# Performance work log

Hardware: AMD Instinct MI355X
Metric: run time of the kernel (lower is better)

## Reference

```python
import math
import jax, jax.numpy as jnp
import numpy as np

D_HEAD = 64
KS = 7
EPS = 1e-6


def _rope_freqs(d_head, n_heads):
    # AxialRoPE buffer: exp(linspace(log(pi), log(10*pi), nh*dim//4+1)[:-1]).view(dim//4, nh).T
    dim = d_head // 2
    n = n_heads * dim // 4
    f = np.exp(np.linspace(math.log(math.pi), math.log(10.0 * math.pi), n + 1)[:-1]).astype(np.float32)
    return jnp.asarray(f.reshape(dim // 4, n_heads).T)  # [nh, dim//4]


def setup_inputs() -> dict:
    key = jax.random.key(0)
    ks = jax.random.split(key, 6)
    B, C, T, H, W = 1, 512, 4, 32, 32
    cond_features = 256
    nh = C // D_HEAD
    x = jax.random.normal(ks[0], (B, C, T, H, W), dtype=jnp.float32)
    pos = jax.random.uniform(ks[1], (B, H, W, 2), dtype=jnp.float32)
    cond = jax.random.normal(ks[2], (B, cond_features), dtype=jnp.float32)
    # zero-init layers in the original (norm.linear, out_proj) get small random weights
    # here so the reference exercises nontrivial math/gradients.
    norm_w = jax.random.normal(ks[3], (cond_features, C), dtype=jnp.float32) * 0.02
    qkv_w = jax.random.normal(ks[4], (C, 3 * C), dtype=jnp.float32) * (1.0 / math.sqrt(C))
    out_w = jax.random.normal(ks[5], (C, C), dtype=jnp.float32) * (1.0 / math.sqrt(C))
    scale = jnp.full((nh,), 10.0, dtype=jnp.float32)
    return {"x": x, "pos": pos, "cond": cond, "norm_w": norm_w, "qkv_w": qkv_w,
            "scale": scale, "out_w": out_w}


def reference(x, pos, cond, norm_w, qkv_w, scale, out_w):
    B, C, T, H, W = x.shape
    nh = C // D_HEAD
    N = B * T
    skip = x

    # b c t h w -> (b t) h w c
    xr = jnp.transpose(x, (0, 2, 3, 4, 1)).reshape(N, H, W, C)
    condr = jnp.repeat(cond, T, axis=0)  # (b t) c, b-major

    # AdaRMSNorm: scale = linear(cond) + 1, applied with rms normalization
    s = condr @ norm_w + 1.0  # [N, C]
    mean_sq = jnp.mean(xr * xr, axis=-1, keepdims=True)
    xn = xr * (s[:, None, None, :] * jax.lax.rsqrt(mean_sq + EPS))

    qkv = (xn @ qkv_w).reshape(N, H, W, 3, nh, D_HEAD)
    q, k, v = qkv[:, :, :, 0], qkv[:, :, :, 1], qkv[:, :, :, 2]  # [N,H,W,nh,e]

    # cosine-sim scaling per head
    sqrt_scale = jnp.sqrt(scale)[:, None]  # [nh,1]
    q = q * (sqrt_scale * jax.lax.rsqrt(jnp.sum(q * q, -1, keepdims=True) + EPS))
    k = k * (sqrt_scale * jax.lax.rsqrt(jnp.sum(k * k, -1, keepdims=True) + EPS))

    # axial RoPE
    freqs = _rope_freqs(D_HEAD, nh)  # [nh, e//8]
    theta = jnp.concatenate([pos[..., None, 0:1] * freqs,
                             pos[..., None, 1:2] * freqs], axis=-1)  # [B,H,W,nh,e//4]
    theta = jnp.repeat(theta, T, axis=0)  # [N,H,W,nh,d]
    d = theta.shape[-1]
    cos_t, sin_t = jnp.cos(theta), jnp.sin(theta)

    def rope(t):
        x1, x2, x3 = t[..., :d], t[..., d:2 * d], t[..., 2 * d:]
        return jnp.concatenate([x1 * cos_t - x2 * sin_t,
                                x2 * cos_t + x1 * sin_t, x3], axis=-1)

    q, k = rope(q), rope(k)

    # neighborhood attention (NATTEN na2d semantics: window clamped to image border)
    r = KS // 2
    ih = jnp.clip(jnp.arange(H) - r, 0, H - KS)[:, None] + jnp.arange(KS)  # [H,KS]
    iw = jnp.clip(jnp.arange(W) - r, 0, W - KS)[:, None] + jnp.arange(KS)  # [W,KS]

    def windows(t):  # [N,H,W,nh,e] -> [N,H,W,KS*KS,nh,e]
        g = t[:, ih[:, :, None, None], iw[None, None, :, :]]  # [N,H,KS,W,KS,nh,e]
        return jnp.transpose(g, (0, 1, 3, 2, 4, 5, 6)).reshape(N, H, W, KS * KS, nh, D_HEAD)

    kw, vw = windows(k), windows(v)
    logits = jnp.einsum('nhwce,nhwkce->nhwck', q, kw)  # scale=1.0 in na2d call
    attn = jax.nn.softmax(logits, axis=-1)
    o = jnp.einsum('nhwck,nhwkce->nhwce', attn, vw).reshape(N, H, W, C)

    y = o @ out_w  # dropout=0.0
    y = jnp.transpose(y.reshape(B, T, H, W, C), (0, 4, 1, 2, 3))
    return y + skip
```

## Files before the change

kernel.cpp:

```cpp
#include <hip/hip_runtime.h>
#include <hip/hip_bf16.h>

typedef __hip_bfloat16 bf16;
#define F32(b) __bfloat162float(b)
#define B16(f) __float2bfloat16(f)

typedef __attribute__((ext_vector_type(8))) short short8;
typedef __attribute__((ext_vector_type(4))) float f32x4;

#define C_DIM 512
#define P_DIM 4096

__device__ __forceinline__ float wave_sum(float v){
#pragma unroll
  for (int o = 32; o > 0; o >>= 1) v += __shfl_xor(v, o, 64);
  return v;
}

__global__ __launch_bounds__(256) void k_prep_s(const float* __restrict__ cond,
                                                const float* __restrict__ norm_w,
                                                float* __restrict__ s){
  __shared__ float red[8][33];
  int c_l = threadIdx.x & 31, fo = threadIdx.x >> 5;
  int c = blockIdx.x * 32 + c_l;
  float acc = 0.f;
  for (int f = fo * 32; f < fo * 32 + 32; ++f)
    acc = fmaf(cond[f], norm_w[f * 512 + c], acc);
  red[fo][c_l] = acc;
  __syncthreads();
  if (threadIdx.x < 32){
    float a = 0.f;
#pragma unroll
    for (int i = 0; i < 8; ++i) a += red[i][c_l];
    s[blockIdx.x * 32 + c_l] = a + 1.0f;
  }
}

__global__ __launch_bounds__(256) void k_rms(const float* __restrict__ x,
                                             float* __restrict__ rms_part){
  __shared__ float red[4][64];
  int bp = blockIdx.x & 63, bc = blockIdx.x >> 6;
  int co = threadIdx.x >> 6, pl = threadIdx.x & 63;
  int p = bp * 64 + pl;
  float acc = 0.f;
  for (int c = bc * 64 + co; c < bc * 64 + 64; c += 4){
    float v = x[c * P_DIM + p];
    acc = fmaf(v, v, acc);
  }
  red[co][pl] = acc;
  __syncthreads();
  if (threadIdx.x < 64){
    int q = threadIdx.x;
    rms_part[bc * P_DIM + bp * 64 + q] = red[0][q] + red[1][q] + red[2][q] + red[3][q];
  }
}

__global__ __launch_bounds__(256) void k_castwT(const float* __restrict__ qkv_w,
                                                const float* __restrict__ out_w,
                                                bf16* __restrict__ qkvT,
                                                bf16* __restrict__ outT){
  __shared__ float tile[64][65];
  int bid = blockIdx.x;
  const float* src; bf16* dst; int NW, n0, c0;
  if (bid < 192){ src = qkv_w; dst = qkvT; NW = 1536; n0 = (bid % 24) * 64; c0 = (bid / 24) * 64; }
  else { int b = bid - 192; src = out_w; dst = outT; NW = 512; n0 = (b & 7) * 64; c0 = (b >> 3) * 64; }
  int grp = threadIdx.x >> 6, lane = threadIdx.x & 63;
  for (int i = grp; i < 64; i += 4)
    tile[i][lane] = src[(c0 + i) * NW + n0 + lane];
  __syncthreads();
  for (int j = grp; j < 64; j += 4)
    dst[(n0 + j) * 512 + c0 + lane] = B16(tile[lane][j]);
}

__global__ __launch_bounds__(256) void k_xnt(const float* __restrict__ x,
                                             const float* __restrict__ s,
                                             const float* __restrict__ rms_part,
                                             bf16* __restrict__ xn){
  __shared__ float tile[64][65];
  int bp = blockIdx.x & 63, bc = blockIdx.x >> 6;
  int p0 = bp * 64, c0 = bc * 64;
  int grp = threadIdx.x >> 6, lane = threadIdx.x & 63;
  for (int i = grp; i < 64; i += 4)
    tile[i][lane] = x[(c0 + i) * P_DIM + p0 + lane] * s[c0 + i];
  __syncthreads();
  for (int j = grp; j < 64; j += 4){
    float ss = 0.f;
#pragma unroll
    for (int i = 0; i < 8; ++i) ss += rms_part[i * P_DIM + p0 + j];
    float rv = rsqrtf(ss * (1.0f / 512.0f) + 1e-6f);
    xn[(size_t)(p0 + j) * 512 + c0 + lane] = B16(tile[lane][j] * rv);
  }
}

#define AS 72
__global__ __launch_bounds__(256) void k_gemm_qkv(const bf16* __restrict__ Ab,
                                                  const bf16* __restrict__ BTb,
                                                  bf16* __restrict__ qkv_bf){
  __shared__ unsigned short a_t[128 * AS];
  __shared__ unsigned short b_t[64 * AS];
  const unsigned short* A  = (const unsigned short*)Ab;
  const unsigned short* BT = (const unsigned short*)BTb;
  int m0 = blockIdx.x * 128;
  int n0 = blockIdx.y * 64;
  int tid = threadIdx.x;
  int w = tid >> 6, l = tid & 63, g = l >> 4, cb = l & 15;

  f32x4 acc[2][4];
#pragma unroll
  for (int mi = 0; mi < 2; ++mi)
#pragma unroll
    for (int nj = 0; nj < 4; ++nj)
#pragma unroll
      for (int r = 0; r < 4; ++r) acc[mi][nj][r] = 0.f;

  for (int kk = 0; kk < 512; kk += 64){
#pragma unroll
    for (int i = 0; i < 4; ++i){
      int sid = tid + i * 256;
      int row = sid >> 3, seg = sid & 7;
      *(uint4*)&a_t[row * AS + seg * 8] = *(const uint4*)&A[(size_t)(m0 + row) * 512 + kk + seg * 8];
    }
#pragma unroll
    for (int i = 0; i < 2; ++i){
      int sid = tid + i * 256;
      int row = sid >> 3, seg = sid & 7;
      *(uint4*)&b_t[row * AS + seg * 8] = *(const uint4*)&BT[(size_t)(n0 + row) * 512 + kk + seg * 8];
    }
    __syncthreads();
#pragma unroll
    for (int kc = 0; kc < 2; ++kc){
      short8 af[2];
#pragma unroll
      for (int mi = 0; mi < 2; ++mi)
        af[mi] = *(const short8*)&a_t[(w * 32 + mi * 16 + cb) * AS + kc * 32 + g * 8];
#pragma unroll
      for (int nj = 0; nj < 4; ++nj){
        short8 bfr = *(const short8*)&b_t[(nj * 16 + cb) * AS + kc * 32 + g * 8];
#pragma unroll
        for (int mi = 0; mi < 2; ++mi)
          acc[mi][nj] = __builtin_amdgcn_mfma_f32_16x16x32_bf16(af[mi], bfr, acc[mi][nj], 0, 0, 0);
      }
    }
    __syncthreads();
  }
#pragma unroll
  for (int mi = 0; mi < 2; ++mi)
#pragma unroll
    for (int nj = 0; nj < 4; ++nj){
      int col = n0 + nj * 16 + cb;
#pragma unroll
      for (int r = 0; r < 4; ++r){
        int rowg = m0 + w * 32 + mi * 16 + g * 4 + r;
        qkv_bf[(size_t)rowg * 1536 + col] = B16(acc[mi][nj][r]);
      }
    }
}

__global__ __launch_bounds__(256) void k_normrope(bf16* __restrict__ qkv_bf,
                                                  const float* __restrict__ scale,
                                                  const float* __restrict__ pos){
  int u = blockIdx.x * 4 + (threadIdx.x >> 6);
  int d = threadIdx.x & 63;
  int p = u >> 4;
  int r = u & 15;
  int head = r >> 1;
  int qk = r & 1;
  size_t base = (size_t)p * 1536 + qk * 512 + head * 64;
  float v = F32(qkv_bf[base + d]);
  float ss = wave_sum(v * v);
  v *= sqrtf(scale[head]) * rsqrtf(ss + 1e-6f);
  float partner = __shfl_xor(v, 16, 64);
  int j = d & 15;
  int axis = j >> 3, i = j & 7;
  const float LOG_PI = 1.1447298858494002f;
  const float LOG10F = 2.302585092994046f;
  float f = __expf(LOG_PI + (float)(i * 8 + head) * (LOG10F / 64.0f));
  float th = pos[(p & 1023) * 2 + axis] * f;
  float ct = __cosf(th), st = __sinf(th);
  float outv;
  if (d < 16)       outv = v * ct - partner * st;
  else if (d < 32)  outv = v * ct + partner * st;
  else              outv = v;
  qkv_bf[base + d] = B16(outv);
}

#define KL_S 80
#define VT_S 232
#define PP_S 232
__global__ __launch_bounds__(256) void k_attn(const bf16* __restrict__ qkv_bfp,
                                              bf16* __restrict__ o_bf){
  __shared__ unsigned short kp[208 * KL_S];
  __shared__ unsigned short vT[64 * VT_S];
  const unsigned short* qkv = (const unsigned short*)qkv_bfp;

  int bid = blockIdx.x;
  int head = bid & 7;
  int patch = bid >> 3;
  int t = patch >> 4;
  int ph = (patch >> 2) & 3, pw = patch & 3;
  int h0 = ph * 8, w0 = pw * 8;
  int rs = min(max(h0 - 3, 0), 18);
  int cs = min(max(w0 - 3, 0), 18);
  int tbase = t << 10;
  int tid = threadIdx.x;
  int cp = tid & 31, pxg = tid >> 5;

  for (int i = 0; i < 26; ++i){
    int px = i * 8 + pxg;
    unsigned val = 0;
    if (px < 196){
      int rr = px / 14, cc = px - rr * 14;
      size_t pn = (size_t)(tbase + (rs + rr) * 32 + (cs + cc));
      val = *(const unsigned*)&qkv[pn * 1536 + 512 + head * 64 + cp * 2];
    }
    *(unsigned*)&kp[px * KL_S + cp * 2] = val;
  }
  for (int i = 0; i < 14; ++i){
    int pp = i * 8 + pxg;
    int px0 = 2 * pp, px1 = px0 + 1;
    unsigned v0 = 0, v1 = 0;
    if (px0 < 196){
      int rr = px0 / 14, cc = px0 - rr * 14;
      size_t pn = (size_t)(tbase + (rs + rr) * 32 + (cs + cc));
      v0 = *(const unsigned*)&qkv[pn * 1536 + 1024 + head * 64 + cp * 2];
    }
    if (px1 < 196){
      int rr = px1 / 14, cc = px1 - rr * 14;
      size_t pn = (size_t)(tbase + (rs + rr) * 32 + (cs + cc));
      v1 = *(const unsigned*)&qkv[pn * 1536 + 1024 + head * 64 + cp * 2];
    }
    unsigned lo = (v0 & 0xffffu) | (v1 << 16);
    unsigned hi = (v0 >> 16) | (v1 & 0xffff0000u);
    *(unsigned*)&vT[(2 * cp) * VT_S + 2 * pp] = lo;
    *(unsigned*)&vT[(2 * cp + 1) * VT_S + 2 * pp] = hi;
  }

  int w = tid >> 6, l = tid & 63;
  int g = l >> 4, cb = l & 15;

  int q_a = w * 16 + cb;
  size_t abase = (size_t)(tbase + (h0 + (q_a >> 3)) * 32 + (w0 + (q_a & 7))) * 1536 + head * 64;
  short8 qa0 = *(const short8*)&qkv[abase + g * 8];
  short8 qa1 = *(const short8*)&qkv[abase + 32 + g * 8];

  __syncthreads();

  f32x4 acc[13];
#pragma unroll
  for (int nt = 0; nt < 13; ++nt)
#pragma unroll
    for (int r = 0; r < 4; ++r) acc[nt][r] = 0.f;
#pragma unroll
  for (int nt = 0; nt < 13; ++nt){
    short8 kb0 = *(const short8*)&kp[(nt * 16 + cb) * KL_S + g * 8];
    short8 kb1 = *(const short8*)&kp[(nt * 16 + cb) * KL_S + 32 + g * 8];
    acc[nt] = __builtin_amdgcn_mfma_f32_16x16x32_bf16(qa0, kb0, acc[nt], 0, 0, 0);
    acc[nt] = __builtin_amdgcn_mfma_f32_16x16x32_bf16(qa1, kb1, acc[nt], 0, 0, 0);
  }
  __syncthreads();

  int wr0[4], wc0[4];
#pragma unroll
  for (int r = 0; r < 4; ++r){
    int q_l = w * 16 + g * 4 + r;
    int hq = h0 + (q_l >> 3), wq = w0 + (q_l & 7);
    wr0[r] = min(max(hq - 3, 0), 25) - rs;
    wc0[r] = min(max(wq - 3, 0), 25) - cs;
  }
  float mx[4] = {-1e30f, -1e30f, -1e30f, -1e30f};
#pragma unroll
  for (int nt = 0; nt < 13; ++nt){
    int kg = nt * 16 + cb;
    int kr = kg / 14, kc = kg - kr * 14;
    bool kvalid = kg < 196;
#pragma unroll
    for (int r = 0; r < 4; ++r){
      bool v = kvalid && ((unsigned)(kr - wr0[r]) < 7u) && ((unsigned)(kc - wc0[r]) < 7u);
      float lg = v ? acc[nt][r] : -1e30f;
      acc[nt][r] = lg;
      mx[r] = fmaxf(mx[r], lg);
    }
  }
#pragma unroll
  for (int off = 1; off < 16; off <<= 1)
#pragma unroll
    for (int r = 0; r < 4; ++r) mx[r] = fmaxf(mx[r], __shfl_xor(mx[r], off, 64));
  float sm[4] = {0.f, 0.f, 0.f, 0.f};
#pragma unroll
  for (int nt = 0; nt < 13; ++nt)
#pragma unroll
    for (int r = 0; r < 4; ++r){
      float e = __expf(acc[nt][r] - mx[r]);
      acc[nt][r] = e;
      sm[r] += e;
    }
#pragma unroll
  for (int off = 1; off < 16; off <<= 1)
#pragma unroll
    for (int r = 0; r < 4; ++r) sm[r] += __shfl_xor(sm[r], off, 64);
  float inv[4];
#pragma unroll
  for (int r = 0; r < 4; ++r) inv[r] = 1.0f / sm[r];

#pragma unroll
  for (int nt = 0; nt < 13; ++nt)
#pragma unroll
    for (int r = 0; r < 4; ++r)
      *reinterpret_cast<bf16*>(&kp[(w * 16 + g * 4 + r) * PP_S + nt * 16 + cb]) = B16(acc[nt][r] * inv[r]);
#pragma unroll
  for (int r = 0; r < 4; ++r)
    kp[(w * 16 + g * 4 + r) * PP_S + 208 + cb] = 0;
  __syncthreads();

  f32x4 acc2[4];
#pragma unroll
  for (int ct = 0; ct < 4; ++ct)
#pragma unroll
    for (int r = 0; r < 4; ++r) acc2[ct][r] = 0.f;
#pragma unroll
  for (int kt = 0; kt < 7; ++kt){
    short8 pa = *(const short8*)&kp[(w * 16 + cb) * PP_S + kt * 32 + g * 8];
#pragma unroll
    for (int ct = 0; ct < 4; ++ct){
      short8 vb = *(const short8*)&vT[(ct * 16 + cb) * VT_S + kt * 32 + g * 8];
      acc2[ct] = __builtin_amdgcn_mfma_f32_16x16x32_bf16(pa, vb, acc2[ct], 0, 0, 0);
    }
  }
#pragma unroll
  for (int ct = 0; ct < 4; ++ct)
#pragma unroll
    for (int r = 0; r < 4; ++r){
      int q_l = w * 16 + g * 4 + r;
      int p = tbase + (h0 + (q_l >> 3)) * 32 + (w0 + (q_l & 7));
      o_bf[(size_t)p * 512 + head * 64 + ct * 16 + cb] = B16(acc2[ct][r]);
    }
}

__global__ __launch_bounds__(256) void k_gemm_out(const bf16* __restrict__ Ab,
                                                  const bf16* __restrict__ BTb,
                                                  const float* __restrict__ xres,
                                                  float* __restrict__ out){
  __shared__ unsigned short a_t[128 * AS];
  __shared__ unsigned short b_t[64 * AS];
  __shared__ float tile[64][65];
  const unsigned short* A  = (const unsigned short*)Ab;
  const unsigned short* BT = (const unsigned short*)BTb;
  int m0 = blockIdx.x * 128;
  int n0 = blockIdx.y * 64;
  int tid = threadIdx.x;
  int w = tid >> 6, l = tid & 63, g = l >> 4, cb = l & 15;

  f32x4 acc[2][4];
#pragma unroll
  for (int mi = 0; mi < 2; ++mi)
#pragma unroll
    for (int nj = 0; nj < 4; ++nj)
#pragma unroll
      for (int r = 0; r < 4; ++r) acc[mi][nj][r] = 0.f;

  for (int kk = 0; kk < 512; kk += 64){
#pragma unroll
    for (int i = 0; i < 4; ++i){
      int sid = tid + i * 256;
      int row = sid >> 3, seg = sid & 7;
      *(uint4*)&a_t[row * AS + seg * 8] = *(const uint4*)&A[(size_t)(m0 + row) * 512 + kk + seg * 8];
    }
#pragma unroll
    for (int i = 0; i < 2; ++i){
      int sid = tid + i * 256;
      int row = sid >> 3, seg = sid & 7;
      *(uint4*)&b_t[row * AS + seg * 8] = *(const uint4*)&BT[(size_t)(n0 + row) * 512 + kk + seg * 8];
    }
    __syncthreads();
#pragma unroll
    for (int kc = 0; kc < 2; ++kc){
      short8 af[2];
#pragma unroll
      for (int mi = 0; mi < 2; ++mi)
        af[mi] = *(const short8*)&a_t[(w * 32 + mi * 16 + cb) * AS + kc * 32 + g * 8];
#pragma unroll
      for (int nj = 0; nj < 4; ++nj){
        short8 bfr = *(const short8*)&b_t[(nj * 16 + cb) * AS + kc * 32 + g * 8];
#pragma unroll
        for (int mi = 0; mi < 2; ++mi)
          acc[mi][nj] = __builtin_amdgcn_mfma_f32_16x16x32_bf16(af[mi], bfr, acc[mi][nj], 0, 0, 0);
      }
    }
    __syncthreads();
  }
  int grp = tid >> 6, lane = tid & 63;
#pragma unroll
  for (int hh = 0; hh < 2; ++hh){
    __syncthreads();
    if ((w >> 1) == hh){
#pragma unroll
      for (int mi = 0; mi < 2; ++mi)
#pragma unroll
        for (int nj = 0; nj < 4; ++nj)
#pragma unroll
          for (int r = 0; r < 4; ++r)
            tile[(w & 1) * 32 + mi * 16 + g * 4 + r][nj * 16 + cb] = acc[mi][nj][r];
    }
    __syncthreads();
    for (int j2 = grp; j2 < 64; j2 += 4){
      int c = n0 + j2;
      int p = m0 + hh * 64 + lane;
      out[(size_t)c * P_DIM + p] = tile[lane][j2] + xres[(size_t)c * P_DIM + p];
    }
  }
}

extern "C" void kernel_launch(void* const* d_in, const int* in_sizes, int n_in,
                              void* d_out, int out_size, void* d_ws, size_t ws_size,
                              hipStream_t stream){
  const float* x      = (const float*)d_in[0];
  const float* pos    = (const float*)d_in[1];
  const float* cond   = (const float*)d_in[2];
  const float* norm_w = (const float*)d_in[3];
  const float* qkv_w  = (const float*)d_in[4];
  const float* scale  = (const float*)d_in[5];
  const float* out_w  = (const float*)d_in[6];
  float* out = (float*)d_out;

  char* wp = (char*)d_ws;
  auto alloc = [&](size_t bytes) -> char* {
    char* r = wp;
    wp += (bytes + 255) & ~((size_t)255);
    return r;
  };
  float* s_f      = (float*)alloc(512 * 4);
  float* rms_part = (float*)alloc(8 * 4096 * 4);
  bf16*  xn       = (bf16*) alloc((size_t)4096 * 512 * 2);
  bf16*  qkvT     = (bf16*) alloc((size_t)1536 * 512 * 2);
  bf16*  outT     = (bf16*) alloc((size_t)512 * 512 * 2);
  bf16*  qkv_bf   = (bf16*) alloc((size_t)4096 * 1536 * 2);
  bf16*  o_bf     = (bf16*) alloc((size_t)4096 * 512 * 2);

  k_prep_s  <<<16,          256, 0, stream>>>(cond, norm_w, s_f);
  k_rms     <<<512,         256, 0, stream>>>(x, rms_part);
  k_castwT  <<<256,         256, 0, stream>>>(qkv_w, out_w, qkvT, outT);
  k_xnt     <<<512,         256, 0, stream>>>(x, s_f, rms_part, xn);
  k_gemm_qkv<<<dim3(32,24), 256, 0, stream>>>(xn, qkvT, qkv_bf);
  k_normrope<<<16384,       256, 0, stream>>>(qkv_bf, scale, pos);
  k_attn    <<<512,         256, 0, stream>>>(qkv_bf, o_bf);
  k_gemm_out<<<dim3(32,8),  256, 0, stream>>>(o_bf, outT, x, out);
}
```

Before: 155.1 us.

## Fuse q/k cosine norm and RoPE into QKV GEMM epilogue; merge prep kernels

Moves the per-head L2 normalization, scale and axial RoPE into the QKV GEMM epilogue, working on fp32 accumulators. Each head is a 64-wide N tile, so the row sum-of-squares is a 16-lane shuffle reduction. This removes the separate normrope kernel and its bf16 read-modify-write of q/k. It also merges the three small prep kernels (cond linear, RMS partials, weight transpose-cast) into one launch with block-range dispatch. The main cost is extra epilogue work on two-thirds of the GEMM tiles. A side effect is that normalization now happens before bf16 rounding rather than after.

```diff
diff --git a/kernel.cpp b/kernel.cpp
--- a/kernel.cpp
+++ b/kernel.cpp
@@ -11,65 +11,58 @@
 #define C_DIM 512
 #define P_DIM 4096
 
-__device__ __forceinline__ float wave_sum(float v){
-#pragma unroll
-  for (int o = 32; o > 0; o >>= 1) v += __shfl_xor(v, o, 64);
-  return v;
-}
-
-__global__ __launch_bounds__(256) void k_prep_s(const float* __restrict__ cond,
-                                                const float* __restrict__ norm_w,
-                                                float* __restrict__ s){
-  __shared__ float red[8][33];
-  int c_l = threadIdx.x & 31, fo = threadIdx.x >> 5;
-  int c = blockIdx.x * 32 + c_l;
-  float acc = 0.f;
-  for (int f = fo * 32; f < fo * 32 + 32; ++f)
-    acc = fmaf(cond[f], norm_w[f * 512 + c], acc);
-  red[fo][c_l] = acc;
-  __syncthreads();
-  if (threadIdx.x < 32){
-    float a = 0.f;
-#pragma unroll
-    for (int i = 0; i < 8; ++i) a += red[i][c_l];
-    s[blockIdx.x * 32 + c_l] = a + 1.0f;
-  }
-}
-
-__global__ __launch_bounds__(256) void k_rms(const float* __restrict__ x,
-                                             float* __restrict__ rms_part){
-  __shared__ float red[4][64];
-  int bp = blockIdx.x & 63, bc = blockIdx.x >> 6;
-  int co = threadIdx.x >> 6, pl = threadIdx.x & 63;
-  int p = bp * 64 + pl;
-  float acc = 0.f;
-  for (int c = bc * 64 + co; c < bc * 64 + 64; c += 4){
-    float v = x[c * P_DIM + p];
-    acc = fmaf(v, v, acc);
-  }
-  red[co][pl] = acc;
-  __syncthreads();
-  if (threadIdx.x < 64){
-    int q = threadIdx.x;
-    rms_part[bc * P_DIM + bp * 64 + q] = red[0][q] + red[1][q] + red[2][q] + red[3][q];
-  }
-}
-
-__global__ __launch_bounds__(256) void k_castwT(const float* __restrict__ qkv_w,
-                                                const float* __restrict__ out_w,
-                                                bf16* __restrict__ qkvT,
-                                                bf16* __restrict__ outT){
-  __shared__ float tile[64][65];
+__global__ __launch_bounds__(256) void k_prep(const float* __restrict__ cond,
+                                              const float* __restrict__ norm_w,
+                                              const float* __restrict__ x,
+                                              const float* __restrict__ qkv_w,
+                                              const float* __restrict__ out_w,
+                                              float* __restrict__ s,
+                                              float* __restrict__ rms_part,
+                                              bf16* __restrict__ qkvT,
+                                              bf16* __restrict__ outT){
+  __shared__ float sh[64 * 65];
   int bid = blockIdx.x;
-  const float* src; bf16* dst; int NW, n0, c0;
-  if (bid < 192){ src = qkv_w; dst = qkvT; NW = 1536; n0 = (bid % 24) * 64; c0 = (bid / 24) * 64; }
-  else { int b = bid - 192; src = out_w; dst = outT; NW = 512; n0 = (b & 7) * 64; c0 = (b >> 3) * 64; }
-  int grp = threadIdx.x >> 6, lane = threadIdx.x & 63;
-  for (int i = grp; i < 64; i += 4)
-    tile[i][lane] = src[(c0 + i) * NW + n0 + lane];
-  __syncthreads();
-  for (int j = grp; j < 64; j += 4)
-    dst[(n0 + j) * 512 + c0 + lane] = B16(tile[lane][j]);
+  int tid = threadIdx.x;
+  if (bid < 16){
+    int c_l = tid & 31, fo = tid >> 5;
+    int c = bid * 32 + c_l;
+    float acc = 0.f;
+    for (int f = fo * 32; f < fo * 32 + 32; ++f)
+      acc = fmaf(cond[f], norm_w[f * 512 + c], acc);
+    sh[fo * 33 + c_l] = acc;
+    __syncthreads();
+    if (tid < 32){
+      float a = 0.f;
+#pragma unroll
+      for (int i = 0; i < 8; ++i) a += sh[i * 33 + tid];
+      s[bid * 32 + tid] = a + 1.0f;
+    }
+  } else if (bid < 528){
+    int b = bid - 16;
+    int bp = b & 63, bc = b >> 6;
+    int co = tid >> 6, pl = tid & 63;
+    int p = bp * 64 + pl;
+    float acc = 0.f;
+    for (int c = bc * 64 + co; c < bc * 64 + 64; c += 4){
+      float v = x[c * P_DIM + p];
+      acc = fmaf(v, v, acc);
+    }
+    sh[co * 64 + pl] = acc;
+    __syncthreads();
+    if (tid < 64)
+      rms_part[bc * P_DIM + bp * 64 + tid] = sh[tid] + sh[64 + tid] + sh[128 + tid] + sh[192 + tid];
+  } else {
+    int b = bid - 528;
+    const float* src; bf16* dst; int NW, n0, c0;
+    if (b < 192){ src = qkv_w; dst = qkvT; NW = 1536; n0 = (b % 24) * 64; c0 = (b / 24) * 64; }
+    else { int bb = b - 192; src = out_w; dst = outT; NW = 512; n0 = (bb & 7) * 64; c0 = (bb >> 3) * 64; }
+    int grp = tid >> 6, lane = tid & 63;
+    for (int i = grp; i < 64; i += 4)
+      sh[i * 65 + lane] = src[(c0 + i) * NW + n0 + lane];
+    __syncthreads();
+    for (int j = grp; j < 64; j += 4)
+      dst[(n0 + j) * 512 + c0 + lane] = B16(sh[lane * 65 + j]);
+  }
 }
 
 __global__ __launch_bounds__(256) void k_xnt(const float* __restrict__ x,
@@ -95,13 +88,16 @@
 #define AS 72
 __global__ __launch_bounds__(256) void k_gemm_qkv(const bf16* __restrict__ Ab,
                                                   const bf16* __restrict__ BTb,
+                                                  const float* __restrict__ scale,
+                                                  const float* __restrict__ pos,
                                                   bf16* __restrict__ qkv_bf){
   __shared__ unsigned short a_t[128 * AS];
   __shared__ unsigned short b_t[64 * AS];
   const unsigned short* A  = (const unsigned short*)Ab;
   const unsigned short* BT = (const unsigned short*)BTb;
   int m0 = blockIdx.x * 128;
-  int n0 = blockIdx.y * 64;
+  int by = blockIdx.y;
+  int n0 = by * 64;
   int tid = threadIdx.x;
   int w = tid >> 6, l = tid & 63, g = l >> 4, cb = l & 15;
 
@@ -143,6 +139,35 @@
     }
     __syncthreads();
   }
+
+  if (by < 16){
+    int head = by & 7;
+    float sqs = sqrtf(scale[head]);
+    int axis = cb >> 3, i = cb & 7;
+    const float LOG_PI = 1.1447298858494002f;
+    const float LOG10F = 2.302585092994046f;
+    float f = __expf(LOG_PI + (float)(i * 8 + head) * (LOG10F / 64.0f));
+#pragma unroll
+    for (int mi = 0; mi < 2; ++mi)
+#pragma unroll
+      for (int r = 0; r < 4; ++r){
+        float ss = 0.f;
+#pragma unroll
+        for (int nj = 0; nj < 4; ++nj) ss = fmaf(acc[mi][nj][r], acc[mi][nj][r], ss);
+#pragma unroll
+        for (int off = 1; off < 16; off <<= 1) ss += __shfl_xor(ss, off, 64);
+        float fac = sqs * rsqrtf(ss + 1e-6f);
+        int rowg = m0 + w * 32 + mi * 16 + g * 4 + r;
+        float th = pos[(rowg & 1023) * 2 + axis] * f;
+        float ct = __cosf(th), st = __sinf(th);
+        float v0 = acc[mi][0][r] * fac, v1 = acc[mi][1][r] * fac;
+        acc[mi][0][r] = v0 * ct - v1 * st;
+        acc[mi][1][r] = v1 * ct + v0 * st;
+        acc[mi][2][r] *= fac;
+        acc[mi][3][r] *= fac;
+      }
+  }
+
 #pragma unroll
   for (int mi = 0; mi < 2; ++mi)
 #pragma unroll
@@ -154,34 +179,6 @@
         qkv_bf[(size_t)rowg * 1536 + col] = B16(acc[mi][nj][r]);
       }
     }
-}
-
-__global__ __launch_bounds__(256) void k_normrope(bf16* __restrict__ qkv_bf,
-                                                  const float* __restrict__ scale,
-                                                  const float* __restrict__ pos){
-  int u = blockIdx.x * 4 + (threadIdx.x >> 6);
-  int d = threadIdx.x & 63;
-  int p = u >> 4;
-  int r = u & 15;
-  int head = r >> 1;
-  int qk = r & 1;
-  size_t base = (size_t)p * 1536 + qk * 512 + head * 64;
-  float v = F32(qkv_bf[base + d]);
-  float ss = wave_sum(v * v);
-  v *= sqrtf(scale[head]) * rsqrtf(ss + 1e-6f);
-  float partner = __shfl_xor(v, 16, 64);
-  int j = d & 15;
-  int axis = j >> 3, i = j & 7;
-  const float LOG_PI = 1.1447298858494002f;
-  const float LOG10F = 2.302585092994046f;
-  float f = __expf(LOG_PI + (float)(i * 8 + head) * (LOG10F / 64.0f));
-  float th = pos[(p & 1023) * 2 + axis] * f;
-  float ct = __cosf(th), st = __sinf(th);
-  float outv;
-  if (d < 16)       outv = v * ct - partner * st;
-  else if (d < 32)  outv = v * ct + partner * st;
-  else              outv = v;
-  qkv_bf[base + d] = B16(outv);
 }
 
 #define KL_S 80
@@ -436,12 +433,10 @@
   bf16*  qkv_bf   = (bf16*) alloc((size_t)4096 * 1536 * 2);
   bf16*  o_bf     = (bf16*) alloc((size_t)4096 * 512 * 2);
 
-  k_prep_s  <<<16,          256, 0, stream>>>(cond, norm_w, s_f);
-  k_rms     <<<512,         256, 0, stream>>>(x, rms_part);
-  k_castwT  <<<256,         256, 0, stream>>>(qkv_w, out_w, qkvT, outT);
+  k_prep    <<<784,         256, 0, stream>>>(cond, norm_w, x, qkv_w, out_w,
+                                              s_f, rms_part, qkvT, outT);
   k_xnt     <<<512,         256, 0, stream>>>(x, s_f, rms_part, xn);
-  k_gemm_qkv<<<dim3(32,24), 256, 0, stream>>>(xn, qkvT, qkv_bf);
-  k_normrope<<<16384,       256, 0, stream>>>(qkv_bf, scale, pos);
+  k_gemm_qkv<<<dim3(32,24), 256, 0, stream>>>(xn, qkvT, scale, pos, qkv_bf);
   k_attn    <<<512,         256, 0, stream>>>(qkv_bf, o_bf);
   k_gemm_out<<<dim3(32,8),  256, 0, stream>>>(o_bf, outT, x, out);
 }
```

New measurement: 130.5 us. 1.19x faster.
